# Optimization experiments

Measured on AMD Instinct MI355X. Metric: run time of the kernel, lower is better.

The kernel has to match this reference:

```python
import jax, jax.numpy as jnp
import numpy as np

KNN = 8

def setup_inputs() -> dict:
    key = jax.random.key(0)
    ks = jax.random.split(key, 6)
    B, C, H, W = 4, 256, 512, 256
    c_red, K = 64, 64
    g_in = C // c_red   # 4 input channels per group in reduce
    g_out = C // c_red  # 4 output channels per group in expand
    stdv = 1.0 / np.sqrt(c_red)
    return {
        "x": jax.random.normal(ks[0], (B, C, H, W), dtype=jnp.float32),
        "Uk": jax.random.normal(ks[1], (B, H, K), dtype=jnp.float32),
        "W_reduce": jax.random.normal(ks[2], (c_red, g_in), dtype=jnp.float32) * 0.1,
        "W_gcn": jax.random.uniform(ks[3], (c_red, c_red), jnp.float32, -stdv, stdv),
        "b_gcn": jax.random.uniform(ks[4], (c_red,), jnp.float32, -stdv, stdv),
        "W_expand": jax.random.normal(ks[5], (c_red, g_out), dtype=jnp.float32) * 0.1,
    }

def reference(x, Uk, W_reduce, W_gcn, b_gcn, W_expand):
    B, C, H, W = x.shape
    c_red, g_in = W_reduce.shape
    g_out = W_expand.shape[1]

    # node features: mean over width -> [B, C, H]
    Xn = x.mean(axis=3)
    # grouped 1x1 conv reduce: [B, c_red, g_in, H] x [c_red, g_in] -> [B, H, c_red]
    Xr = jnp.einsum('bogh,og->bho', Xn.reshape(B, c_red, g_in, H), W_reduce)

    # batched KNN adjacency from cosine similarity of Uk rows
    norm = jnp.maximum(jnp.linalg.norm(Uk, axis=-1, keepdims=True), 1e-12)
    U = Uk / norm                                   # [B, H, K]
    sim = jnp.einsum('bhk,bgk->bhg', U, U)          # [B, H, H]
    vals, idx = jax.lax.top_k(sim, min(KNN, H))     # [B, H, k]
    deg = vals.sum(axis=-1)                         # row-sum degree [B, H]
    dinv = deg ** -0.5
    b_ix = jnp.arange(B)[:, None, None]
    vals_n = vals * dinv[:, :, None] * dinv[b_ix, idx]  # sym-normalized edge weights

    # GCN: support = X W ; out = A_norm @ support + bias ; relu
    support = jnp.einsum('bhc,cd->bhd', Xr, W_gcn)      # [B, H, c_red]
    neigh = support[b_ix, idx]                          # [B, H, k, c_red] gather
    out = jnp.einsum('bhk,bhkc->bhc', vals_n, neigh) + b_gcn
    out = jax.nn.relu(out)

    # grouped 1x1 conv expand: [B, H, c_red] -> [B, C, H]
    exp = jnp.einsum('bhg,gj->bgjh', out, W_expand).reshape(B, C, H)
    # broadcast across width
    return jnp.broadcast_to(exp[..., None], (B, C, H, W))
```

## Files before the change

kernel.cpp:

```cpp
#include <hip/hip_runtime.h>
#include <math.h>

#define BB 4
#define CC 256
#define HH 512
#define WW 256
#define CRED 64
#define GIN 4
#define KNN8 8

typedef float f4 __attribute__((ext_vector_type(4)));

__device__ __forceinline__ float wave_sum(float v) {
#pragma unroll
    for (int off = 32; off; off >>= 1) v += __shfl_xor(v, off, 64);
    return v;
}

__global__ __launch_bounds__(256) void mean_reduce_kernel(const float* __restrict__ x,
                                                          const float* __restrict__ Wr,
                                                          float* __restrict__ Xr) {
    int wgid = (blockIdx.x * 256 + threadIdx.x) >> 6;
    int lane = threadIdx.x & 63;
#pragma unroll
    for (int it = 0; it < 16; ++it) {
        int row = wgid + (it << 13);
        int h = row & 511;
        int o = (row >> 9) & 63;
        int b = row >> 15;
        float s = 0.f;
#pragma unroll
        for (int g = 0; g < GIN; ++g) {
            const f4 v = __builtin_nontemporal_load(
                (const f4*)(x + ((size_t)((b * CC + o * GIN + g) * HH + h)) * WW + lane * 4));
            s += Wr[o * GIN + g] * (v.x + v.y + v.z + v.w);
        }
        s = wave_sum(s);
        if (lane == 0) Xr[((((b << 9) + h) << 6)) + o] = s * (1.f / 256.f);
    }
}

__global__ __launch_bounds__(256) void normalize_kernel(const float* __restrict__ Uk,
                                                        float* __restrict__ Un) {
    int gid  = blockIdx.x * 256 + threadIdx.x;
    int wid  = gid >> 6;
    int lane = threadIdx.x & 63;
    float v  = Uk[wid * 64 + lane];
    float ss = wave_sum(v * v);
    float norm = fmaxf(sqrtf(ss), 1e-12f);
    Un[wid * 64 + lane] = v / norm;
}

__global__ __launch_bounds__(256) void topk_kernel(const float* __restrict__ Un,
                                                   float* __restrict__ topv,
                                                   int* __restrict__ topi,
                                                   float* __restrict__ deg) {
    int gid  = blockIdx.x * 256 + threadIdx.x;
    int wid  = gid >> 6;
    int lane = threadIdx.x & 63;
    int b = wid >> 9;
    const float* Ub = Un + b * HH * 64;
    const float* uh = Un + wid * 64;

    float sim[8];
#pragma unroll
    for (int j = 0; j < 8; ++j) sim[j] = 0.f;
#pragma unroll 4
    for (int kk = 0; kk < 64; ++kk) {
        float uhv = uh[kk];
#pragma unroll
        for (int j = 0; j < 8; ++j) sim[j] += uhv * Ub[(lane + 64 * j) * 64 + kk];
    }

    float vsum = 0.f;
#pragma unroll
    for (int r = 0; r < KNN8; ++r) {
        float bv = sim[0]; int bj = 0;
#pragma unroll
        for (int j = 1; j < 8; ++j) { if (sim[j] > bv) { bv = sim[j]; bj = j; } }
        float v = bv; int g = lane + 64 * bj;
#pragma unroll
        for (int off = 32; off; off >>= 1) {
            float ov = __shfl_xor(v, off, 64);
            int   og = __shfl_xor(g, off, 64);
            if (ov > v || (ov == v && og < g)) { v = ov; g = og; }
        }
        vsum += v;
        if (lane == 0) { topv[wid * KNN8 + r] = v; topi[wid * KNN8 + r] = g; }
        if ((g & 63) == lane) sim[g >> 6] = -INFINITY;
    }
    if (lane == 0) deg[wid] = vsum;
}

__global__ __launch_bounds__(64) void gcnval_kernel(const float* __restrict__ Xr,
                                                    const float* __restrict__ Wg,
                                                    const float* __restrict__ bg,
                                                    const float* __restrict__ topv,
                                                    const int* __restrict__ topi,
                                                    const float* __restrict__ deg,
                                                    float* __restrict__ yout) {
    int bh   = blockIdx.x;
    int b    = bh >> 9;
    int lane = threadIdx.x & 63;

    float dh = 1.0f / sqrtf(deg[bh]);
    float z = 0.f;
#pragma unroll
    for (int k = 0; k < KNN8; ++k) {
        int   i = topi[bh * KNN8 + k];
        float w = topv[bh * KNN8 + k] * dh * (1.0f / sqrtf(deg[(b << 9) + i]));
        z += w * Xr[(((b << 9) + i) << 6) + lane];
    }
    float y = 0.f;
#pragma unroll 16
    for (int c = 0; c < CRED; ++c) y += __shfl(z, c, 64) * Wg[c * CRED + lane];
    yout[(bh << 6) + lane] = fmaxf(y + bg[lane], 0.f);
}

__global__ __launch_bounds__(256) void out_kernel(const float* __restrict__ yout,
                                                  const float* __restrict__ We,
                                                  float* __restrict__ out) {
    int gid = blockIdx.x * 256 + threadIdx.x;
    int row = gid >> 6;
    int w4  = gid & 63;
    int h = row & 511;
    int c = (row >> 9) & 255;
    int b = row >> 17;
    float val = yout[(((b << 9) + h) << 6) + (c >> 2)] * We[c];
    f4 v = {val, val, val, val};
    __builtin_nontemporal_store(v, (f4*)(out + (size_t)row * WW + w4 * 4));
}

extern "C" void kernel_launch(void* const* d_in, const int* in_sizes, int n_in,
                              void* d_out, int out_size, void* d_ws, size_t ws_size,
                              hipStream_t stream) {
    const float* x  = (const float*)d_in[0];
    const float* Uk = (const float*)d_in[1];
    const float* Wr = (const float*)d_in[2];
    const float* Wg = (const float*)d_in[3];
    const float* bg = (const float*)d_in[4];
    const float* We = (const float*)d_in[5];
    float* out = (float*)d_out;
    float* ws  = (float*)d_ws;

    float* Xr   = ws;
    float* Un   = ws + 131072;
    float* topv = ws + 262144;
    int*   topi = (int*)(ws + 278528);
    float* deg  = ws + 294912;
    float* yout = ws + 296960;

    hipLaunchKernelGGL(mean_reduce_kernel, dim3(2048),   dim3(256), 0, stream, x, Wr, Xr);
    hipLaunchKernelGGL(normalize_kernel,   dim3(512),    dim3(256), 0, stream, Uk, Un);
    hipLaunchKernelGGL(topk_kernel,        dim3(512),    dim3(256), 0, stream, Un, topv, topi, deg);
    hipLaunchKernelGGL(gcnval_kernel,      dim3(2048),   dim3(64),  0, stream, Xr, Wg, bg, topv, topi, deg, yout);
    hipLaunchKernelGGL(out_kernel,         dim3(131072), dim3(256), 0, stream, yout, We, out);
}
```

Measured before the change: 239.9 us.

## Split mean-reduce into contiguous row-mean pass and small grouped reduce kernel

The fused mean+grouped-reduce kernel, which had each wave loop over 16 strided row groups, is replaced by two kernels. A row-mean kernel launches one wave per contiguous 1 KB row of x and writes per-row means to a new workspace buffer. A small grouped-reduce kernel then applies the 4-wide reduce weights. This gives the streaming read of x more parallelism and simpler addressing, at the cost of an extra kernel launch and a small intermediate buffer.

```diff
diff --git a/kernel.cpp b/kernel.cpp
--- a/kernel.cpp
+++ b/kernel.cpp
@@ -17,27 +17,29 @@
     return v;
 }
 
-__global__ __launch_bounds__(256) void mean_reduce_kernel(const float* __restrict__ x,
-                                                          const float* __restrict__ Wr,
-                                                          float* __restrict__ Xr) {
-    int wgid = (blockIdx.x * 256 + threadIdx.x) >> 6;
+__global__ __launch_bounds__(256) void rowmean_kernel(const float* __restrict__ x,
+                                                      float* __restrict__ M) {
+    int gid  = blockIdx.x * 256 + threadIdx.x;
+    int row  = gid >> 6;
     int lane = threadIdx.x & 63;
+    const f4 v = __builtin_nontemporal_load((const f4*)(x + (size_t)row * WW + lane * 4));
+    float s = wave_sum(v.x + v.y + v.z + v.w);
+    if (lane == 0) M[row] = s * (1.f / 256.f);
+}
+
+__global__ __launch_bounds__(256) void greduce_kernel(const float* __restrict__ M,
+                                                      const float* __restrict__ Wr,
+                                                      float* __restrict__ Xr) {
+    int gid  = blockIdx.x * 256 + threadIdx.x;
+    int wid  = gid >> 6;
+    int lane = threadIdx.x & 63;
+    int b = wid >> 9, h = wid & 511;
+    const float* Mb = M + (size_t)b * CC * HH;
+    float s = 0.f;
 #pragma unroll
-    for (int it = 0; it < 16; ++it) {
-        int row = wgid + (it << 13);
-        int h = row & 511;
-        int o = (row >> 9) & 63;
-        int b = row >> 15;
-        float s = 0.f;
-#pragma unroll
-        for (int g = 0; g < GIN; ++g) {
-            const f4 v = __builtin_nontemporal_load(
-                (const f4*)(x + ((size_t)((b * CC + o * GIN + g) * HH + h)) * WW + lane * 4));
-            s += Wr[o * GIN + g] * (v.x + v.y + v.z + v.w);
-        }
-        s = wave_sum(s);
-        if (lane == 0) Xr[((((b << 9) + h) << 6)) + o] = s * (1.f / 256.f);
-    }
+    for (int g = 0; g < GIN; ++g)
+        s += Wr[lane * GIN + g] * Mb[(lane * GIN + g) * HH + h];
+    Xr[(wid << 6) + lane] = s;
 }
 
 __global__ __launch_bounds__(256) void normalize_kernel(const float* __restrict__ Uk,
@@ -149,10 +151,12 @@
     int*   topi = (int*)(ws + 278528);
     float* deg  = ws + 294912;
     float* yout = ws + 296960;
+    float* M    = ws + 428032;
 
-    hipLaunchKernelGGL(mean_reduce_kernel, dim3(2048),   dim3(256), 0, stream, x, Wr, Xr);
-    hipLaunchKernelGGL(normalize_kernel,   dim3(512),    dim3(256), 0, stream, Uk, Un);
-    hipLaunchKernelGGL(topk_kernel,        dim3(512),    dim3(256), 0, stream, Un, topv, topi, deg);
-    hipLaunchKernelGGL(gcnval_kernel,      dim3(2048),   dim3(64),  0, stream, Xr, Wg, bg, topv, topi, deg, yout);
-    hipLaunchKernelGGL(out_kernel,         dim3(131072), dim3(256), 0, stream, yout, We, out);
+    hipLaunchKernelGGL(normalize_kernel, dim3(512),    dim3(256), 0, stream, Uk, Un);
+    hipLaunchKernelGGL(rowmean_kernel,   dim3(131072), dim3(256), 0, stream, x, M);
+    hipLaunchKernelGGL(greduce_kernel,   dim3(512),    dim3(256), 0, stream, M, Wr, Xr);
+    hipLaunchKernelGGL(topk_kernel,      dim3(512),    dim3(256), 0, stream, Un, topv, topi, deg);
+    hipLaunchKernelGGL(gcnval_kernel,    dim3(2048),   dim3(64),  0, stream, Xr, Wg, bg, topv, topi, deg, yout);
+    hipLaunchKernelGGL(out_kernel,       dim3(131072), dim3(256), 0, stream, yout, We, out);
 }
```

Measured after the change: 269.1 us. 1.12x slower.
